# Kernel optimization log

Hardware: AMD Instinct MI355X
Metric: run time of the kernel (lower is better)

Reference implementation:

```python
import jax, jax.numpy as jnp
import numpy as np

N = 50000      # nodes
E = 800000     # edges (before self-loops)
IN = 256       # input features
H = 8          # heads
C = 32         # hidden channels per head
OUT = 40       # classes
NEG_SLOPE = 0.2


def setup_inputs() -> dict:
    key = jax.random.key(0)
    ks = jax.random.split(key, 12)
    sd = lambda k, sh: (jax.random.normal(k, sh, jnp.float32) * 0.05)
    return {
        "x": jax.random.normal(ks[0], (N, IN), jnp.float32),
        "edge_index": jax.random.randint(ks[1], (2, E), 0, N),
        "W1": sd(ks[2], (IN, H * C)),
        "a_src1": sd(ks[3], (H, C)),
        "a_dst1": sd(ks[4], (H, C)),
        "b1": jnp.zeros((C,), jnp.float32),
        "W2": sd(ks[5], (C, H * C)),
        "a_src2": sd(ks[6], (H, C)),
        "a_dst2": sd(ks[7], (H, C)),
        "b2": jnp.zeros((C,), jnp.float32),
        "Wo": sd(ks[8], (C, OUT)),
        "bo": jnp.zeros((OUT,), jnp.float32),
    }


def gat_layer(x, src, dst, n, W, a_src, a_dst, b):
    # x: [N, F]; src/dst: [E'] (self-loops included). concat=False -> mean over heads.
    h = (x @ W).reshape(n, H, C)                       # [N, H, C]
    alpha_src = jnp.sum(h * a_src, axis=-1)            # [N, H]
    alpha_dst = jnp.sum(h * a_dst, axis=-1)            # [N, H]
    e = alpha_src[src] + alpha_dst[dst]                # [E', H]
    e = jnp.where(e > 0, e, NEG_SLOPE * e)             # leaky_relu
    # segment softmax over incoming edges of each dst node
    m = jax.ops.segment_max(e, dst, num_segments=n)    # [N, H]
    ex = jnp.exp(e - m[dst])                           # [E', H]
    s = jax.ops.segment_sum(ex, dst, num_segments=n)   # [N, H]
    alpha = ex / s[dst]                                # [E', H]
    msg = alpha[:, :, None] * h[src]                   # [E', H, C]
    out = jax.ops.segment_sum(msg, dst, num_segments=n)  # [N, H, C]
    return out.mean(axis=1) + b                        # [N, C]


def reference(x, edge_index, W1, a_src1, a_dst1, b1, W2, a_src2, a_dst2, b2, Wo, bo):
    n = x.shape[0]
    loops = jnp.arange(n, dtype=edge_index.dtype)
    src = jnp.concatenate([edge_index[0], loops])      # add self-loops (PyG default)
    dst = jnp.concatenate([edge_index[1], loops])
    h = gat_layer(x, src, dst, n, W1, a_src1, a_dst1, b1)
    h = jax.nn.elu(h)                                  # dropout skipped (eval)
    h = gat_layer(h, src, dst, n, W2, a_src2, a_dst2, b2)
    h = jax.nn.elu(h)
    logits = h @ Wo + bo
    return jax.nn.log_softmax(logits, axis=1)
```

## Files before the change

### kernel.cpp

```cpp
#include <hip/hip_runtime.h>
#include <math.h>

#define N_NODES 50000
#define N_PAD   50016
#define N_EDGES 800000
#define E_TOT   (N_EDGES + N_NODES)
#define F_IN    256
#define NHEAD   8
#define CH      32
#define HC      256
#define OUT_C   40
#define NEG_SLOPE 0.2f
#define CAP     64
#define G_WCVT  ((HC * F_IN + 255) / 256)
#define G_WCVT2 ((HC * CH + 255) / 256)
#define NRANGE  8
#define RANGE_SZ (N_NODES / NRANGE)
#define BIN_CHUNK 2048
#define G_BINCH ((E_TOT + BIN_CHUNK - 1) / BIN_CHUNK)
#define G_BIN   (G_BINCH * NRANGE)

typedef unsigned short u16;
typedef unsigned int   u32;
typedef unsigned char  u8;
typedef __attribute__((ext_vector_type(8))) short bf16x8;
typedef __attribute__((ext_vector_type(4))) float f32x4;
typedef __attribute__((ext_vector_type(2))) float f32x2;

__device__ __forceinline__ u16 f2bf(float f) {
    union { u32 u; float f; } x; x.f = f;
    u32 u = x.u;
    return (u16)((u + 0x7fffu + ((u >> 16) & 1u)) >> 16);
}
__device__ __forceinline__ float bflo(u32 v) {
    union { u32 u; float f; } x; x.u = v << 16; return x.f;
}
__device__ __forceinline__ u8 f2fp8(float f) {
    return (u8)(__builtin_amdgcn_cvt_pk_fp8_f32(f, f, 0, false) & 0xff);
}


__global__ __launch_bounds__(256) void prep_kernel(const int* __restrict__ ei,
        int* __restrict__ cursor, u16* __restrict__ csr_src,
        const float* __restrict__ W1, u16* __restrict__ Wt,
        const float* __restrict__ W2, u16* __restrict__ W2t) {
    int b = blockIdx.x;
    if (b < G_BIN) {
        const int r  = b & (NRANGE - 1);
        const int ch = b >> 3;
        const int lo = r * RANGE_SZ, hi = lo + RANGE_SZ;
        int j0 = ch * BIN_CHUNK + threadIdx.x;
        #pragma unroll
        for (int i = 0; i < BIN_CHUNK / 256; ++i) {
            int j = j0 + i * 256;
            if (j < E_TOT) {
                int d = (j < N_EDGES) ? ei[N_EDGES + j] : (j - N_EDGES);
                if (d >= lo && d < hi) {
                    int s = (j < N_EDGES) ? ei[j] : d;
                    int pos = atomicAdd(&cursor[d], 1);
                    if (pos < CAP) csr_src[d * CAP + pos] = (u16)s;
                }
            }
        }
    } else if (b < G_BIN + G_WCVT) {
        int t = (b - G_BIN) * 256 + threadIdx.x;
        int n = t & 255, k = t >> 8;
        Wt[(size_t)n * F_IN + k] = f2bf(W1[(size_t)k * HC + n]);
    } else {
        int t = (b - G_BIN - G_WCVT) * 256 + threadIdx.x;
        if (t >= HC * CH) return;
        int n = t & 255, k = t >> 8;
        W2t[(size_t)n * CH + k] = f2bf(W2[(size_t)k * HC + n]);
    }
}

__global__ __launch_bounds__(256) void sort_kernel(const int* __restrict__ cursor,
        u16* __restrict__ csr_src) {
    const int dst  = (blockIdx.x * 256 + threadIdx.x) >> 6;
    if (dst >= N_NODES) return;
    const int lane = threadIdx.x & 63;
    const int cnt  = min(cursor[dst], CAP);
    u32 v = (lane < cnt) ? (u32)csr_src[dst * CAP + lane] : 0x7FFFFFFFu;
    #pragma unroll
    for (int k = 2; k <= 64; k <<= 1) {
        #pragma unroll
        for (int j = k >> 1; j > 0; j >>= 1) {
            u32 pv = (u32)__shfl_xor((int)v, j, 64);
            bool asc      = ((lane & k) == 0);
            bool keep_min = (((lane & j) == 0) == asc);
            v = keep_min ? min(v, pv) : max(v, pv);
        }
    }
    if (lane < cnt) csr_src[dst * CAP + lane] = (u16)v;
}

__device__ __forceinline__ void gemm_epilogue(f32x4 acc[2][4], int row0, int quad,
        int l16, int nb, const float* __restrict__ a_src,
        const float* __restrict__ a_dst, u8* __restrict__ ht8,
        float* __restrict__ asrc, float* __restrict__ adst) {
    #pragma unroll
    for (int m = 0; m < 2; ++m) {
        #pragma unroll
        for (int r = 0; r < 4; ++r) {
            int row = row0 + m * 16 + quad * 4 + r;
            if (row < N_NODES) {
                u8* hr = ht8 + (size_t)row * HC;
                #pragma unroll
                for (int n = 0; n < 4; ++n)
                    hr[nb + n * 16 + l16] = f2fp8(acc[m][n][r]);
            }
        }
    }
    const int hA = nb >> 5;
    const float sA0 = a_src[hA * 32 + l16],       sA1 = a_src[hA * 32 + 16 + l16];
    const float sB0 = a_src[(hA + 1) * 32 + l16], sB1 = a_src[(hA + 1) * 32 + 16 + l16];
    const float dA0 = a_dst[hA * 32 + l16],       dA1 = a_dst[hA * 32 + 16 + l16];
    const float dB0 = a_dst[(hA + 1) * 32 + l16], dB1 = a_dst[(hA + 1) * 32 + 16 + l16];
    #pragma unroll
    for (int m = 0; m < 2; ++m) {
        #pragma unroll
        for (int r = 0; r < 4; ++r) {
            float pa = acc[m][0][r] * sA0 + acc[m][1][r] * sA1;
            float pb = acc[m][2][r] * sB0 + acc[m][3][r] * sB1;
            float qa = acc[m][0][r] * dA0 + acc[m][1][r] * dA1;
            float qb = acc[m][2][r] * dB0 + acc[m][3][r] * dB1;
            #pragma unroll
            for (int off = 1; off < 16; off <<= 1) {
                pa += __shfl_xor(pa, off, 64);
                pb += __shfl_xor(pb, off, 64);
                qa += __shfl_xor(qa, off, 64);
                qb += __shfl_xor(qb, off, 64);
            }
            int row = row0 + m * 16 + quad * 4 + r;
            if (l16 == 0 && row < N_NODES) {
                asrc[row * NHEAD + hA]     = pa;
                asrc[row * NHEAD + hA + 1] = pb;
                adst[row * NHEAD + hA]     = qa;
                adst[row * NHEAD + hA + 1] = qb;
            }
        }
    }
}

__global__ __launch_bounds__(256) void gemm1_mfma(const float* __restrict__ x,
        const u16* __restrict__ Wt, const float* __restrict__ a_src,
        const float* __restrict__ a_dst, u8* __restrict__ ht8,
        float* __restrict__ asrc, float* __restrict__ adst) {
    __shared__ u16 As[32 * 256];
    const int row0 = blockIdx.x * 32;
    const int t    = threadIdx.x;

    {
        const int r   = t >> 3;
        const int sub = t & 7;
        const int gr  = min(row0 + r, N_NODES - 1);
        const float4* xr = (const float4*)(x + (size_t)gr * F_IN);
        const int sw = (r & 7) << 4;
        char* Ar = (char*)As + r * 512;
        #pragma unroll
        for (int i = 0; i < 8; ++i) {
            int f4 = i * 8 + sub;
            float4 v = xr[f4];
            u32 lo = (u32)f2bf(v.x) | ((u32)f2bf(v.y) << 16);
            u32 hi = (u32)f2bf(v.z) | ((u32)f2bf(v.w) << 16);
            *(uint2*)(Ar + ((f4 * 8) ^ sw)) = make_uint2(lo, hi);
        }
    }
    __syncthreads();

    const int wave = t >> 6;
    const int lane = t & 63;
    const int l16  = lane & 15;
    const int quad = lane >> 4;
    const int nb   = wave * 64;
    const int swr  = (l16 & 7) << 4;
    const char* Ab = (const char*)As;

    f32x4 acc[2][4];
    #pragma unroll
    for (int m = 0; m < 2; ++m)
        #pragma unroll
        for (int n = 0; n < 4; ++n) acc[m][n] = (f32x4){0.f, 0.f, 0.f, 0.f};

    const u16* bp = Wt + (size_t)(nb + l16) * F_IN;

    #pragma unroll 1
    for (int k0 = 0; k0 < F_IN; k0 += 32) {
        const int ko = k0 + quad * 8;
        bf16x8 a0 = *(const bf16x8*)(Ab + l16 * 512 + ((ko * 2) ^ swr));
        bf16x8 a1 = *(const bf16x8*)(Ab + (16 + l16) * 512 + ((ko * 2) ^ swr));
        bf16x8 b0 = *(const bf16x8*)(bp + 0 * 16 * F_IN + ko);
        bf16x8 b1 = *(const bf16x8*)(bp + 1 * 16 * F_IN + ko);
        bf16x8 b2 = *(const bf16x8*)(bp + 2 * 16 * F_IN + ko);
        bf16x8 b3 = *(const bf16x8*)(bp + 3 * 16 * F_IN + ko);
        acc[0][0] = __builtin_amdgcn_mfma_f32_16x16x32_bf16(a0, b0, acc[0][0], 0, 0, 0);
        acc[0][1] = __builtin_amdgcn_mfma_f32_16x16x32_bf16(a0, b1, acc[0][1], 0, 0, 0);
        acc[0][2] = __builtin_amdgcn_mfma_f32_16x16x32_bf16(a0, b2, acc[0][2], 0, 0, 0);
        acc[0][3] = __builtin_amdgcn_mfma_f32_16x16x32_bf16(a0, b3, acc[0][3], 0, 0, 0);
        acc[1][0] = __builtin_amdgcn_mfma_f32_16x16x32_bf16(a1, b0, acc[1][0], 0, 0, 0);
        acc[1][1] = __builtin_amdgcn_mfma_f32_16x16x32_bf16(a1, b1, acc[1][1], 0, 0, 0);
        acc[1][2] = __builtin_amdgcn_mfma_f32_16x16x32_bf16(a1, b2, acc[1][2], 0, 0, 0);
        acc[1][3] = __builtin_amdgcn_mfma_f32_16x16x32_bf16(a1, b3, acc[1][3], 0, 0, 0);
    }
    gemm_epilogue(acc, row0, quad, l16, nb, a_src, a_dst, ht8, asrc, adst);
}

__global__ __launch_bounds__(256) void gemm2_mfma(const u16* __restrict__ hmb,
        const u16* __restrict__ W2t, const float* __restrict__ a_src,
        const float* __restrict__ a_dst, u8* __restrict__ ht8,
        float* __restrict__ asrc, float* __restrict__ adst) {
    const int row0 = blockIdx.x * 32;
    const int t    = threadIdx.x;
    const int wave = t >> 6;
    const int lane = t & 63;
    const int l16  = lane & 15;
    const int quad = lane >> 4;
    const int nb   = wave * 64;
    const int ko   = quad * 8;

    const u16* a0p = hmb + (size_t)(row0 + l16) * CH;
    const u16* a1p = a0p + 16 * CH;
    const u16* bp  = W2t + (size_t)(nb + l16) * CH;

    bf16x8 a0 = *(const bf16x8*)(a0p + ko);
    bf16x8 a1 = *(const bf16x8*)(a1p + ko);
    bf16x8 b0 = *(const bf16x8*)(bp + 0 * 16 * CH + ko);
    bf16x8 b1 = *(const bf16x8*)(bp + 1 * 16 * CH + ko);
    bf16x8 b2 = *(const bf16x8*)(bp + 2 * 16 * CH + ko);
    bf16x8 b3 = *(const bf16x8*)(bp + 3 * 16 * CH + ko);

    f32x4 z = (f32x4){0.f, 0.f, 0.f, 0.f};
    f32x4 acc[2][4];
    acc[0][0] = __builtin_amdgcn_mfma_f32_16x16x32_bf16(a0, b0, z, 0, 0, 0);
    acc[0][1] = __builtin_amdgcn_mfma_f32_16x16x32_bf16(a0, b1, z, 0, 0, 0);
    acc[0][2] = __builtin_amdgcn_mfma_f32_16x16x32_bf16(a0, b2, z, 0, 0, 0);
    acc[0][3] = __builtin_amdgcn_mfma_f32_16x16x32_bf16(a0, b3, z, 0, 0, 0);
    acc[1][0] = __builtin_amdgcn_mfma_f32_16x16x32_bf16(a1, b0, z, 0, 0, 0);
    acc[1][1] = __builtin_amdgcn_mfma_f32_16x16x32_bf16(a1, b1, z, 0, 0, 0);
    acc[1][2] = __builtin_amdgcn_mfma_f32_16x16x32_bf16(a1, b2, z, 0, 0, 0);
    acc[1][3] = __builtin_amdgcn_mfma_f32_16x16x32_bf16(a1, b3, z, 0, 0, 0);

    gemm_epilogue(acc, row0, quad, l16, nb, a_src, a_dst, ht8, asrc, adst);
}

__global__ __launch_bounds__(256) void attn_kernel(const int* __restrict__ degp,
        const u16* __restrict__ csr_src, const float* __restrict__ asrc,
        const float* __restrict__ adst, const u8* __restrict__ ht8,
        const float* __restrict__ b, u16* __restrict__ out) {
    const int wid = (blockIdx.x * 256 + threadIdx.x) >> 6;
    if (wid >= N_NODES) return;
    const int dst  = wid;
    const int lane = threadIdx.x & 63;
    const int q    = lane >> 4;
    const int l16  = lane & 15;
    const int h    = l16 >> 1;
    const float ad_own = adst[dst * NHEAD + h];
    const u8* hbase = ht8 + l16 * 16;

    f32x2 acc2[8];
    #pragma unroll
    for (int i = 0; i < 8; ++i) acc2[i] = (f32x2){0.f, 0.f};
    float wsum = 0.f;

    const int cnt = min(degp[dst], CAP);
    const int p0 = dst * CAP, p1 = p0 + cnt;
    const int nt = (cnt + 7) >> 3;

    float asA = -1e30f, asB = -1e30f;
    uint4 hvA = make_uint4(0u, 0u, 0u, 0u), hvB = make_uint4(0u, 0u, 0u, 0u);
    int e = p0 + q;
    if (e < p1) {
        int s = (int)csr_src[e];
        asA = asrc[s * NHEAD + h];
        hvA = *(const uint4*)(hbase + ((size_t)s << 8));
    }
    if (e + 4 < p1) {
        int s = (int)csr_src[e + 4];
        asB = asrc[s * NHEAD + h];
        hvB = *(const uint4*)(hbase + ((size_t)s << 8));
    }

    for (int it = 0; it < nt; ++it) {
        float aA = asA; uint4 hA = hvA;
        float aB = asB; uint4 hB = hvB;
        asA = -1e30f; asB = -1e30f;
        if (e + 8 < p1) {
            int s = (int)csr_src[e + 8];
            asA = asrc[s * NHEAD + h];
            hvA = *(const uint4*)(hbase + ((size_t)s << 8));
        }
        if (e + 12 < p1) {
            int s = (int)csr_src[e + 12];
            asB = asrc[s * NHEAD + h];
            hvB = *(const uint4*)(hbase + ((size_t)s << 8));
        }
        {
            float x = aA + ad_own;
            x = x > 0.f ? x : NEG_SLOPE * x;
            float w = __expf(x);
            wsum += w;
            f32x2 w2; w2.x = w; w2.y = w;
            acc2[0] = __builtin_elementwise_fma(w2, __builtin_amdgcn_cvt_pk_f32_fp8(hA.x, false), acc2[0]);
            acc2[1] = __builtin_elementwise_fma(w2, __builtin_amdgcn_cvt_pk_f32_fp8(hA.x, true ), acc2[1]);
            acc2[2] = __builtin_elementwise_fma(w2, __builtin_amdgcn_cvt_pk_f32_fp8(hA.y, false), acc2[2]);
            acc2[3] = __builtin_elementwise_fma(w2, __builtin_amdgcn_cvt_pk_f32_fp8(hA.y, true ), acc2[3]);
            acc2[4] = __builtin_elementwise_fma(w2, __builtin_amdgcn_cvt_pk_f32_fp8(hA.z, false), acc2[4]);
            acc2[5] = __builtin_elementwise_fma(w2, __builtin_amdgcn_cvt_pk_f32_fp8(hA.z, true ), acc2[5]);
            acc2[6] = __builtin_elementwise_fma(w2, __builtin_amdgcn_cvt_pk_f32_fp8(hA.w, false), acc2[6]);
            acc2[7] = __builtin_elementwise_fma(w2, __builtin_amdgcn_cvt_pk_f32_fp8(hA.w, true ), acc2[7]);
        }
        {
            float x = aB + ad_own;
            x = x > 0.f ? x : NEG_SLOPE * x;
            float w = __expf(x);
            wsum += w;
            f32x2 w2; w2.x = w; w2.y = w;
            acc2[0] = __builtin_elementwise_fma(w2, __builtin_amdgcn_cvt_pk_f32_fp8(hB.x, false), acc2[0]);
            acc2[1] = __builtin_elementwise_fma(w2, __builtin_amdgcn_cvt_pk_f32_fp8(hB.x, true ), acc2[1]);
            acc2[2] = __builtin_elementwise_fma(w2, __builtin_amdgcn_cvt_pk_f32_fp8(hB.y, false), acc2[2]);
            acc2[3] = __builtin_elementwise_fma(w2, __builtin_amdgcn_cvt_pk_f32_fp8(hB.y, true ), acc2[3]);
            acc2[4] = __builtin_elementwise_fma(w2, __builtin_amdgcn_cvt_pk_f32_fp8(hB.z, false), acc2[4]);
            acc2[5] = __builtin_elementwise_fma(w2, __builtin_amdgcn_cvt_pk_f32_fp8(hB.z, true ), acc2[5]);
            acc2[6] = __builtin_elementwise_fma(w2, __builtin_amdgcn_cvt_pk_f32_fp8(hB.w, false), acc2[6]);
            acc2[7] = __builtin_elementwise_fma(w2, __builtin_amdgcn_cvt_pk_f32_fp8(hB.w, true ), acc2[7]);
        }
        e += 8;
    }

    #pragma unroll
    for (int i = 0; i < 8; ++i) {
        acc2[i].x += __shfl_xor(acc2[i].x, 16, 64);
        acc2[i].y += __shfl_xor(acc2[i].y, 16, 64);
        acc2[i].x += __shfl_xor(acc2[i].x, 32, 64);
        acc2[i].y += __shfl_xor(acc2[i].y, 32, 64);
    }
    wsum += __shfl_xor(wsum, 16, 64);
    wsum += __shfl_xor(wsum, 32, 64);

    float winv = 1.0f / wsum;
    f32x2 winv2; winv2.x = winv; winv2.y = winv;
    #pragma unroll
    for (int i = 0; i < 8; ++i) acc2[i] *= winv2;

    #pragma unroll
    for (int i = 0; i < 8; ++i) {
        acc2[i].x += __shfl_xor(acc2[i].x, 2, 64);
        acc2[i].y += __shfl_xor(acc2[i].y, 2, 64);
        acc2[i].x += __shfl_xor(acc2[i].x, 4, 64);
        acc2[i].y += __shfl_xor(acc2[i].y, 4, 64);
        acc2[i].x += __shfl_xor(acc2[i].x, 8, 64);
        acc2[i].y += __shfl_xor(acc2[i].y, 8, 64);
    }

    if (lane < 2) {
        const int c0 = lane * 16;
        const float4* bp4 = (const float4*)(b + c0);
        float4 b0 = bp4[0], b1 = bp4[1], b2 = bp4[2], b3 = bp4[3];
        float bb[16] = {b0.x, b0.y, b0.z, b0.w, b1.x, b1.y, b1.z, b1.w,
                        b2.x, b2.y, b2.z, b2.w, b3.x, b3.y, b3.z, b3.w};
        u32 d[8];
        #pragma unroll
        for (int i = 0; i < 8; ++i) {
            float v0 = acc2[i].x * 0.125f + bb[2 * i];
            float v1 = acc2[i].y * 0.125f + bb[2 * i + 1];
            v0 = v0 > 0.f ? v0 : (__expf(v0) - 1.f);
            v1 = v1 > 0.f ? v1 : (__expf(v1) - 1.f);
            d[i] = (u32)f2bf(v0) | ((u32)f2bf(v1) << 16);
        }
        uint4* op = (uint4*)(out + (size_t)dst * CH + c0);
        op[0] = make_uint4(d[0], d[1], d[2], d[3]);
        op[1] = make_uint4(d[4], d[5], d[6], d[7]);
    }
}

__global__ __launch_bounds__(256) void attn_fin_kernel(const int* __restrict__ degp,
        const u16* __restrict__ csr_src, const float* __restrict__ asrc,
        const float* __restrict__ adst, const u8* __restrict__ ht8,
        const float* __restrict__ b, const float* __restrict__ Wo,
        const float* __restrict__ bo, float* __restrict__ out) {
    const int dst  = (blockIdx.x * 256 + threadIdx.x) >> 6;
    const int lane = threadIdx.x & 63;
    const int w4   = threadIdx.x >> 6;
    const int q    = lane >> 4;
    const int l16  = lane & 15;
    const int h    = l16 >> 1;
    const float ad_own = adst[dst * NHEAD + h];
    const u8* hbase = ht8 + l16 * 16;

    __shared__ float hsm[4][CH];

    f32x2 acc2[8];
    #pragma unroll
    for (int i = 0; i < 8; ++i) acc2[i] = (f32x2){0.f, 0.f};
    float wsum = 0.f;

    const int cnt = min(degp[dst], CAP);
    const int p0 = dst * CAP, p1 = p0 + cnt;
    const int nt = (cnt + 7) >> 3;

    float asA = -1e30f, asB = -1e30f;
    uint4 hvA = make_uint4(0u, 0u, 0u, 0u), hvB = make_uint4(0u, 0u, 0u, 0u);
    int e = p0 + q;
    if (e < p1) {
        int s = (int)csr_src[e];
        asA = asrc[s * NHEAD + h];
        hvA = *(const uint4*)(hbase + ((size_t)s << 8));
    }
    if (e + 4 < p1) {
        int s = (int)csr_src[e + 4];
        asB = asrc[s * NHEAD + h];
        hvB = *(const uint4*)(hbase + ((size_t)s << 8));
    }

    for (int it = 0; it < nt; ++it) {
        float aA = asA; uint4 hA = hvA;
        float aB = asB; uint4 hB = hvB;
        asA = -1e30f; asB = -1e30f;
        if (e + 8 < p1) {
            int s = (int)csr_src[e + 8];
            asA = asrc[s * NHEAD + h];
            hvA = *(const uint4*)(hbase + ((size_t)s << 8));
        }
        if (e + 12 < p1) {
            int s = (int)csr_src[e + 12];
            asB = asrc[s * NHEAD + h];
            hvB = *(const uint4*)(hbase + ((size_t)s << 8));
        }
        {
            float x = aA + ad_own;
            x = x > 0.f ? x : NEG_SLOPE * x;
            float w = __expf(x);
            wsum += w;
            f32x2 w2; w2.x = w; w2.y = w;
            acc2[0] = __builtin_elementwise_fma(w2, __builtin_amdgcn_cvt_pk_f32_fp8(hA.x, false), acc2[0]);
            acc2[1] = __builtin_elementwise_fma(w2, __builtin_amdgcn_cvt_pk_f32_fp8(hA.x, true ), acc2[1]);
            acc2[2] = __builtin_elementwise_fma(w2, __builtin_amdgcn_cvt_pk_f32_fp8(hA.y, false), acc2[2]);
            acc2[3] = __builtin_elementwise_fma(w2, __builtin_amdgcn_cvt_pk_f32_fp8(hA.y, true ), acc2[3]);
            acc2[4] = __builtin_elementwise_fma(w2, __builtin_amdgcn_cvt_pk_f32_fp8(hA.z, false), acc2[4]);
            acc2[5] = __builtin_elementwise_fma(w2, __builtin_amdgcn_cvt_pk_f32_fp8(hA.z, true ), acc2[5]);
            acc2[6] = __builtin_elementwise_fma(w2, __builtin_amdgcn_cvt_pk_f32_fp8(hA.w, false), acc2[6]);
            acc2[7] = __builtin_elementwise_fma(w2, __builtin_amdgcn_cvt_pk_f32_fp8(hA.w, true ), acc2[7]);
        }
        {
            float x = aB + ad_own;
            x = x > 0.f ? x : NEG_SLOPE * x;
            float w = __expf(x);
            wsum += w;
            f32x2 w2; w2.x = w; w2.y = w;
            acc2[0] = __builtin_elementwise_fma(w2, __builtin_amdgcn_cvt_pk_f32_fp8(hB.x, false), acc2[0]);
            acc2[1] = __builtin_elementwise_fma(w2, __builtin_amdgcn_cvt_pk_f32_fp8(hB.x, true ), acc2[1]);
            acc2[2] = __builtin_elementwise_fma(w2, __builtin_amdgcn_cvt_pk_f32_fp8(hB.y, false), acc2[2]);
            acc2[3] = __builtin_elementwise_fma(w2, __builtin_amdgcn_cvt_pk_f32_fp8(hB.y, true ), acc2[3]);
            acc2[4] = __builtin_elementwise_fma(w2, __builtin_amdgcn_cvt_pk_f32_fp8(hB.z, false), acc2[4]);
            acc2[5] = __builtin_elementwise_fma(w2, __builtin_amdgcn_cvt_pk_f32_fp8(hB.z, true ), acc2[5]);
            acc2[6] = __builtin_elementwise_fma(w2, __builtin_amdgcn_cvt_pk_f32_fp8(hB.w, false), acc2[6]);
            acc2[7] = __builtin_elementwise_fma(w2, __builtin_amdgcn_cvt_pk_f32_fp8(hB.w, true ), acc2[7]);
        }
        e += 8;
    }

    #pragma unroll
    for (int i = 0; i < 8; ++i) {
        acc2[i].x += __shfl_xor(acc2[i].x, 16, 64);
        acc2[i].y += __shfl_xor(acc2[i].y, 16, 64);
        acc2[i].x += __shfl_xor(acc2[i].x, 32, 64);
        acc2[i].y += __shfl_xor(acc2[i].y, 32, 64);
    }
    wsum += __shfl_xor(wsum, 16, 64);
    wsum += __shfl_xor(wsum, 32, 64);

    float winv = 1.0f / wsum;
    f32x2 winv2; winv2.x = winv; winv2.y = winv;
    #pragma unroll
    for (int i = 0; i < 8; ++i) acc2[i] *= winv2;

    #pragma unroll
    for (int i = 0; i < 8; ++i) {
        acc2[i].x += __shfl_xor(acc2[i].x, 2, 64);
        acc2[i].y += __shfl_xor(acc2[i].y, 2, 64);
        acc2[i].x += __shfl_xor(acc2[i].x, 4, 64);
        acc2[i].y += __shfl_xor(acc2[i].y, 4, 64);
        acc2[i].x += __shfl_xor(acc2[i].x, 8, 64);
        acc2[i].y += __shfl_xor(acc2[i].y, 8, 64);
    }

    if (lane < 2) {
        #pragma unroll
        for (int i = 0; i < 8; ++i) {
            hsm[w4][lane * 16 + 2 * i]     = acc2[i].x * 0.125f;
            hsm[w4][lane * 16 + 2 * i + 1] = acc2[i].y * 0.125f;
        }
    }
    __syncthreads();
    if (lane < CH) {
        float v = hsm[w4][lane] + b[lane];
        hsm[w4][lane] = v > 0.f ? v : (__expf(v) - 1.f);
    }
    __syncthreads();
    float logit = -INFINITY;
    if (lane < OUT_C) {
        float a = bo[lane];
        #pragma unroll
        for (int k = 0; k < CH; ++k) a += hsm[w4][k] * Wo[k * OUT_C + lane];
        logit = a;
    }
    float mx = logit;
    #pragma unroll
    for (int off = 32; off; off >>= 1) mx = fmaxf(mx, __shfl_xor(mx, off, 64));
    float ex = (lane < OUT_C) ? __expf(logit - mx) : 0.f;
    float ss = ex;
    #pragma unroll
    for (int off = 32; off; off >>= 1) ss += __shfl_xor(ss, off, 64);
    if (lane < OUT_C) out[(size_t)dst * OUT_C + lane] = logit - mx - __logf(ss);
}

extern "C" void kernel_launch(void* const* d_in, const int* in_sizes, int n_in,
                              void* d_out, int out_size, void* d_ws, size_t ws_size,
                              hipStream_t stream) {
    const float* x      = (const float*)d_in[0];
    const int*   ei     = (const int*)  d_in[1];
    const float* W1     = (const float*)d_in[2];
    const float* a_src1 = (const float*)d_in[3];
    const float* a_dst1 = (const float*)d_in[4];
    const float* b1     = (const float*)d_in[5];
    const float* W2     = (const float*)d_in[6];
    const float* a_src2 = (const float*)d_in[7];
    const float* a_dst2 = (const float*)d_in[8];
    const float* b2     = (const float*)d_in[9];
    const float* Wo     = (const float*)d_in[10];
    const float* bo     = (const float*)d_in[11];
    float* out = (float*)d_out;

    char* ws = (char*)d_ws;
    size_t off = 0;
    auto carve = [&](size_t bytes) { char* p = ws + off; off += (bytes + 255) & ~(size_t)255; return p; };
    u8*    ht8     = (u8*)   carve((size_t)N_NODES * HC);
    u16*   Wt      = (u16*)  carve((size_t)HC * F_IN * 2);
    u16*   W2t     = (u16*)  carve((size_t)HC * CH * 2);
    float* asrc    = (float*)carve((size_t)N_NODES * NHEAD * 4);
    float* adst    = (float*)carve((size_t)N_NODES * NHEAD * 4);
    u16*   hmid    = (u16*)  carve((size_t)N_PAD * CH * 2);
    int*   cursor  = (int*)  carve((size_t)N_NODES * 4);
    u16*   csr_src = (u16*)  carve((size_t)N_NODES * CAP * 2);

    const int g_prep  = G_BIN + G_WCVT + G_WCVT2;
    const int g_sort  = (N_NODES * 64 + 255) / 256;
    const int g_gemm  = (N_NODES + 31) / 32;
    const int g_attn  = (N_NODES * 64 + 255) / 256;

    (void)hipMemsetAsync(cursor, 0, (size_t)N_NODES * 4, stream);
    prep_kernel<<<g_prep, 256, 0, stream>>>(ei, cursor, csr_src, W1, Wt, W2, W2t);
    sort_kernel<<<g_sort, 256, 0, stream>>>(cursor, csr_src);

    gemm1_mfma<<<g_gemm, 256, 0, stream>>>(x, Wt, a_src1, a_dst1, ht8, asrc, adst);
    attn_kernel<<<g_attn, 256, 0, stream>>>(cursor, csr_src, asrc, adst, ht8, b1, hmid);

    gemm2_mfma<<<g_gemm, 256, 0, stream>>>(hmid, W2t, a_src2, a_dst2, ht8, asrc, adst);
    attn_fin_kernel<<<g_attn, 256, 0, stream>>>(cursor, csr_src, asrc, adst,
                                                ht8, b2, Wo, bo, out);
}
```

Before: 323.9 us.

## Fuse layer-2 projection into layer-1 attention and drop CSR sort pass

Layer-1 attention now finishes each node by applying ELU, multiplying by W2 (converted to bf16 into shared memory per block), and writing fp8 features plus layer-2 attention logits. This removes the separate gemm2 launch and the hmid round trip. The sort kernel is dropped, so neighbors are visited in atomic-insertion order, and the output projection moves to its own small kernel. Every attention block pays for loading and converting the 16 KB W2 into shared memory. Unsorted neighbor order can change gather locality and make float summation order nondeterministic.

After: 325.8 us. About the same (+0.6%).

```diff
diff --git a/kernel.cpp b/kernel.cpp
--- a/kernel.cpp
+++ b/kernel.cpp
@@ -13,12 +13,12 @@
 #define NEG_SLOPE 0.2f
 #define CAP     64
 #define G_WCVT  ((HC * F_IN + 255) / 256)
-#define G_WCVT2 ((HC * CH + 255) / 256)
 #define NRANGE  8
 #define RANGE_SZ (N_NODES / NRANGE)
 #define BIN_CHUNK 2048
 #define G_BINCH ((E_TOT + BIN_CHUNK - 1) / BIN_CHUNK)
 #define G_BIN   (G_BINCH * NRANGE)
+#define G_GEMM  (N_PAD / 32)
 
 typedef unsigned short u16;
 typedef unsigned int   u32;
@@ -42,8 +42,7 @@
 
 __global__ __launch_bounds__(256) void prep_kernel(const int* __restrict__ ei,
         int* __restrict__ cursor, u16* __restrict__ csr_src,
-        const float* __restrict__ W1, u16* __restrict__ Wt,
-        const float* __restrict__ W2, u16* __restrict__ W2t) {
+        const float* __restrict__ W1, u16* __restrict__ Wt) {
     int b = blockIdx.x;
     if (b < G_BIN) {
         const int r  = b & (NRANGE - 1);
@@ -62,36 +61,11 @@
                 }
             }
         }
-    } else if (b < G_BIN + G_WCVT) {
+    } else {
         int t = (b - G_BIN) * 256 + threadIdx.x;
         int n = t & 255, k = t >> 8;
         Wt[(size_t)n * F_IN + k] = f2bf(W1[(size_t)k * HC + n]);
-    } else {
-        int t = (b - G_BIN - G_WCVT) * 256 + threadIdx.x;
-        if (t >= HC * CH) return;
-        int n = t & 255, k = t >> 8;
-        W2t[(size_t)n * CH + k] = f2bf(W2[(size_t)k * HC + n]);
-    }
-}
-
-__global__ __launch_bounds__(256) void sort_kernel(const int* __restrict__ cursor,
-        u16* __restrict__ csr_src) {
-    const int dst  = (blockIdx.x * 256 + threadIdx.x) >> 6;
-    if (dst >= N_NODES) return;
-    const int lane = threadIdx.x & 63;
-    const int cnt  = min(cursor[dst], CAP);
-    u32 v = (lane < cnt) ? (u32)csr_src[dst * CAP + lane] : 0x7FFFFFFFu;
-    #pragma unroll
-    for (int k = 2; k <= 64; k <<= 1) {
-        #pragma unroll
-        for (int j = k >> 1; j > 0; j >>= 1) {
-            u32 pv = (u32)__shfl_xor((int)v, j, 64);
-            bool asc      = ((lane & k) == 0);
-            bool keep_min = (((lane & j) == 0) == asc);
-            v = keep_min ? min(v, pv) : max(v, pv);
-        }
-    }
-    if (lane < cnt) csr_src[dst * CAP + lane] = (u16)v;
+    }
 }
 
 __device__ __forceinline__ void gemm_epilogue(f32x4 acc[2][4], int row0, int quad,
@@ -205,52 +179,39 @@
     gemm_epilogue(acc, row0, quad, l16, nb, a_src, a_dst, ht8, asrc, adst);
 }
 
-__global__ __launch_bounds__(256) void gemm2_mfma(const u16* __restrict__ hmb,
-        const u16* __restrict__ W2t, const float* __restrict__ a_src,
-        const float* __restrict__ a_dst, u8* __restrict__ ht8,
-        float* __restrict__ asrc, float* __restrict__ adst) {
-    const int row0 = blockIdx.x * 32;
-    const int t    = threadIdx.x;
-    const int wave = t >> 6;
-    const int lane = t & 63;
-    const int l16  = lane & 15;
-    const int quad = lane >> 4;
-    const int nb   = wave * 64;
-    const int ko   = quad * 8;
-
-    const u16* a0p = hmb + (size_t)(row0 + l16) * CH;
-    const u16* a1p = a0p + 16 * CH;
-    const u16* bp  = W2t + (size_t)(nb + l16) * CH;
-
-    bf16x8 a0 = *(const bf16x8*)(a0p + ko);
-    bf16x8 a1 = *(const bf16x8*)(a1p + ko);
-    bf16x8 b0 = *(const bf16x8*)(bp + 0 * 16 * CH + ko);
-    bf16x8 b1 = *(const bf16x8*)(bp + 1 * 16 * CH + ko);
-    bf16x8 b2 = *(const bf16x8*)(bp + 2 * 16 * CH + ko);
-    bf16x8 b3 = *(const bf16x8*)(bp + 3 * 16 * CH + ko);
-
-    f32x4 z = (f32x4){0.f, 0.f, 0.f, 0.f};
-    f32x4 acc[2][4];
-    acc[0][0] = __builtin_amdgcn_mfma_f32_16x16x32_bf16(a0, b0, z, 0, 0, 0);
-    acc[0][1] = __builtin_amdgcn_mfma_f32_16x16x32_bf16(a0, b1, z, 0, 0, 0);
-    acc[0][2] = __builtin_amdgcn_mfma_f32_16x16x32_bf16(a0, b2, z, 0, 0, 0);
-    acc[0][3] = __builtin_amdgcn_mfma_f32_16x16x32_bf16(a0, b3, z, 0, 0, 0);
-    acc[1][0] = __builtin_amdgcn_mfma_f32_16x16x32_bf16(a1, b0, z, 0, 0, 0);
-    acc[1][1] = __builtin_amdgcn_mfma_f32_16x16x32_bf16(a1, b1, z, 0, 0, 0);
-    acc[1][2] = __builtin_amdgcn_mfma_f32_16x16x32_bf16(a1, b2, z, 0, 0, 0);
-    acc[1][3] = __builtin_amdgcn_mfma_f32_16x16x32_bf16(a1, b3, z, 0, 0, 0);
-
-    gemm_epilogue(acc, row0, quad, l16, nb, a_src, a_dst, ht8, asrc, adst);
-}
-
-__global__ __launch_bounds__(256) void attn_kernel(const int* __restrict__ degp,
-        const u16* __restrict__ csr_src, const float* __restrict__ asrc,
-        const float* __restrict__ adst, const u8* __restrict__ ht8,
-        const float* __restrict__ b, u16* __restrict__ out) {
-    const int wid = (blockIdx.x * 256 + threadIdx.x) >> 6;
-    if (wid >= N_NODES) return;
-    const int dst  = wid;
+__global__ __launch_bounds__(256) void attn1_fused_kernel(
+        const int* __restrict__ degp, const u16* __restrict__ csr_src,
+        const float* __restrict__ asrc, const float* __restrict__ adst,
+        const u8* __restrict__ ht8, const float* __restrict__ b1,
+        const float* __restrict__ W2, const float* __restrict__ a_src2,
+        const float* __restrict__ a_dst2, u8* __restrict__ ht8b,
+        float* __restrict__ asrc2, float* __restrict__ adst2) {
+    __shared__ u16  W2s[CH * HC];
+    __shared__ float sas2[HC], sad2[HC];
+    __shared__ float bs1[CH];
+    __shared__ float hrow_s[4][CH];
+
+    {
+        for (int i = threadIdx.x; i < CH * HC / 8; i += 256) {
+            const float4* wp = (const float4*)W2 + (size_t)i * 2;
+            float4 v0 = wp[0], v1 = wp[1];
+            u32 p0 = (u32)f2bf(v0.x) | ((u32)f2bf(v0.y) << 16);
+            u32 p1 = (u32)f2bf(v0.z) | ((u32)f2bf(v0.w) << 16);
+            u32 p2 = (u32)f2bf(v1.x) | ((u32)f2bf(v1.y) << 16);
+            u32 p3 = (u32)f2bf(v1.z) | ((u32)f2bf(v1.w) << 16);
+            ((uint4*)W2s)[i] = make_uint4(p0, p1, p2, p3);
+        }
+        if (threadIdx.x < HC) {
+            sas2[threadIdx.x] = a_src2[threadIdx.x];
+            sad2[threadIdx.x] = a_dst2[threadIdx.x];
+        }
+        if (threadIdx.x < CH) bs1[threadIdx.x] = b1[threadIdx.x];
+    }
+    __syncthreads();
+
+    const int dst  = (blockIdx.x * 256 + threadIdx.x) >> 6;
     const int lane = threadIdx.x & 63;
+    const int w4   = threadIdx.x >> 6;
     const int q    = lane >> 4;
     const int l16  = lane & 15;
     const int h    = l16 >> 1;
@@ -336,12 +297,10 @@
     }
     wsum += __shfl_xor(wsum, 16, 64);
     wsum += __shfl_xor(wsum, 32, 64);
-
     float winv = 1.0f / wsum;
     f32x2 winv2; winv2.x = winv; winv2.y = winv;
     #pragma unroll
     for (int i = 0; i < 8; ++i) acc2[i] *= winv2;
-
     #pragma unroll
     for (int i = 0; i < 8; ++i) {
         acc2[i].x += __shfl_xor(acc2[i].x, 2, 64);
@@ -354,40 +313,60 @@
 
     if (lane < 2) {
         const int c0 = lane * 16;
-        const float4* bp4 = (const float4*)(b + c0);
-        float4 b0 = bp4[0], b1 = bp4[1], b2 = bp4[2], b3 = bp4[3];
-        float bb[16] = {b0.x, b0.y, b0.z, b0.w, b1.x, b1.y, b1.z, b1.w,
-                        b2.x, b2.y, b2.z, b2.w, b3.x, b3.y, b3.z, b3.w};
-        u32 d[8];
         #pragma unroll
         for (int i = 0; i < 8; ++i) {
-            float v0 = acc2[i].x * 0.125f + bb[2 * i];
-            float v1 = acc2[i].y * 0.125f + bb[2 * i + 1];
+            float v0 = acc2[i].x * 0.125f + bs1[c0 + 2 * i];
+            float v1 = acc2[i].y * 0.125f + bs1[c0 + 2 * i + 1];
             v0 = v0 > 0.f ? v0 : (__expf(v0) - 1.f);
             v1 = v1 > 0.f ? v1 : (__expf(v1) - 1.f);
-            d[i] = (u32)f2bf(v0) | ((u32)f2bf(v1) << 16);
-        }
-        uint4* op = (uint4*)(out + (size_t)dst * CH + c0);
-        op[0] = make_uint4(d[0], d[1], d[2], d[3]);
-        op[1] = make_uint4(d[4], d[5], d[6], d[7]);
-    }
-}
-
-__global__ __launch_bounds__(256) void attn_fin_kernel(const int* __restrict__ degp,
+            hrow_s[w4][c0 + 2 * i]     = v0;
+            hrow_s[w4][c0 + 2 * i + 1] = v1;
+        }
+    }
+
+    float o0 = 0.f, o1 = 0.f, o2 = 0.f, o3 = 0.f;
+    const u16* wb = W2s + lane * 4;
+    #pragma unroll
+    for (int k = 0; k < CH; ++k) {
+        uint2 wv = *(const uint2*)(wb + k * HC);
+        float hk = hrow_s[w4][k];
+        o0 += hk * bflo(wv.x & 0xffffu);
+        o1 += hk * bflo(wv.x >> 16);
+        o2 += hk * bflo(wv.y & 0xffffu);
+        o3 += hk * bflo(wv.y >> 16);
+    }
+
+    u32 lo = __builtin_amdgcn_cvt_pk_fp8_f32(o0, o1, 0, false) & 0xffffu;
+    u32 hi = __builtin_amdgcn_cvt_pk_fp8_f32(o2, o3, 0, false) & 0xffffu;
+    *(u32*)(ht8b + (size_t)dst * HC + lane * 4) = lo | (hi << 16);
+
+    const int h2 = lane >> 3;
+    const float* s2 = sas2 + h2 * CH + (lane & 7) * 4;
+    const float* d2 = sad2 + h2 * CH + (lane & 7) * 4;
+    float pa = o0 * s2[0] + o1 * s2[1] + o2 * s2[2] + o3 * s2[3];
+    float qa = o0 * d2[0] + o1 * d2[1] + o2 * d2[2] + o3 * d2[3];
+    pa += __shfl_xor(pa, 1, 64); qa += __shfl_xor(qa, 1, 64);
+    pa += __shfl_xor(pa, 2, 64); qa += __shfl_xor(qa, 2, 64);
+    pa += __shfl_xor(pa, 4, 64); qa += __shfl_xor(qa, 4, 64);
+    if ((lane & 7) == 0) {
+        asrc2[dst * NHEAD + h2] = pa;
+        adst2[dst * NHEAD + h2] = qa;
+    }
+}
+
+__global__ __launch_bounds__(256) void attn_kernel(const int* __restrict__ degp,
         const u16* __restrict__ csr_src, const float* __restrict__ asrc,
         const float* __restrict__ adst, const u8* __restrict__ ht8,
-        const float* __restrict__ b, const float* __restrict__ Wo,
-        const float* __restrict__ bo, float* __restrict__ out) {
-    const int dst  = (blockIdx.x * 256 + threadIdx.x) >> 6;
+        const float* __restrict__ b, u16* __restrict__ out) {
+    const int wid = (blockIdx.x * 256 + threadIdx.x) >> 6;
+    if (wid >= N_NODES) return;
+    const int dst  = wid;
     const int lane = threadIdx.x & 63;
-    const int w4   = threadIdx.x >> 6;
     const int q    = lane >> 4;
     const int l16  = lane & 15;
     const int h    = l16 >> 1;
     const float ad_own = adst[dst * NHEAD + h];
     const u8* hbase = ht8 + l16 * 16;
-
-    __shared__ float hsm[4][CH];
 
     f32x2 acc2[8];
     #pragma unroll
@@ -485,33 +464,51 @@
     }
 
     if (lane < 2) {
+        const int c0 = lane * 16;
+        const float4* bp4 = (const float4*)(b + c0);
+        float4 b0 = bp4[0], b1 = bp4[1], b2 = bp4[2], b3 = bp4[3];
+        float bb[16] = {b0.x, b0.y, b0.z, b0.w, b1.x, b1.y, b1.z, b1.w,
+                        b2.x, b2.y, b2.z, b2.w, b3.x, b3.y, b3.z, b3.w};
+        u32 d[8];
         #pragma unroll
         for (int i = 0; i < 8; ++i) {
-            hsm[w4][lane * 16 + 2 * i]     = acc2[i].x * 0.125f;
-            hsm[w4][lane * 16 + 2 * i + 1] = acc2[i].y * 0.125f;
-        }
-    }
+            float v0 = acc2[i].x * 0.125f + bb[2 * i];
+            float v1 = acc2[i].y * 0.125f + bb[2 * i + 1];
+            v0 = v0 > 0.f ? v0 : (__expf(v0) - 1.f);
+            v1 = v1 > 0.f ? v1 : (__expf(v1) - 1.f);
+            d[i] = (u32)f2bf(v0) | ((u32)f2bf(v1) << 16);
+        }
+        uint4* op = (uint4*)(out + (size_t)dst * CH + c0);
+        op[0] = make_uint4(d[0], d[1], d[2], d[3]);
+        op[1] = make_uint4(d[4], d[5], d[6], d[7]);
+    }
+}
+
+__global__ __launch_bounds__(256) void out_kernel(const u16* __restrict__ hf,
+        const float* __restrict__ Wo, const float* __restrict__ bo,
+        float* __restrict__ out) {
+    const int wave = threadIdx.x >> 6;
+    const int lane = threadIdx.x & 63;
+    const int n    = blockIdx.x * 4 + wave;
+    __shared__ float hs[4][CH];
+    if (n < N_NODES && lane < CH) hs[wave][lane] = bflo((u32)hf[n * CH + lane]);
     __syncthreads();
-    if (lane < CH) {
-        float v = hsm[w4][lane] + b[lane];
-        hsm[w4][lane] = v > 0.f ? v : (__expf(v) - 1.f);
-    }
-    __syncthreads();
+    if (n >= N_NODES) return;
     float logit = -INFINITY;
     if (lane < OUT_C) {
         float a = bo[lane];
         #pragma unroll
-        for (int k = 0; k < CH; ++k) a += hsm[w4][k] * Wo[k * OUT_C + lane];
+        for (int k = 0; k < CH; ++k) a += hs[wave][k] * Wo[k * OUT_C + lane];
         logit = a;
     }
-    float mx = logit;
-    #pragma unroll
-    for (int off = 32; off; off >>= 1) mx = fmaxf(mx, __shfl_xor(mx, off, 64));
-    float ex = (lane < OUT_C) ? __expf(logit - mx) : 0.f;
-    float ss = ex;
-    #pragma unroll
-    for (int off = 32; off; off >>= 1) ss += __shfl_xor(ss, off, 64);
-    if (lane < OUT_C) out[(size_t)dst * OUT_C + lane] = logit - mx - __logf(ss);
+    float m = logit;
+    #pragma unroll
+    for (int off = 32; off; off >>= 1) m = fmaxf(m, __shfl_xor(m, off, 64));
+    float ex = (lane < OUT_C) ? __expf(logit - m) : 0.f;
+    float ssum = ex;
+    #pragma unroll
+    for (int off = 32; off; off >>= 1) ssum += __shfl_xor(ssum, off, 64);
+    if (lane < OUT_C) out[(size_t)n * OUT_C + lane] = logit - m - __logf(ssum);
 }
 
 extern "C" void kernel_launch(void* const* d_in, const int* in_sizes, int n_in,
@@ -534,28 +531,31 @@
     char* ws = (char*)d_ws;
     size_t off = 0;
     auto carve = [&](size_t bytes) { char* p = ws + off; off += (bytes + 255) & ~(size_t)255; return p; };
-    u8*    ht8     = (u8*)   carve((size_t)N_NODES * HC);
+    u8*    ht8a    = (u8*)   carve((size_t)N_NODES * HC);
+    u8*    ht8b    = (u8*)   carve((size_t)N_NODES * HC);
     u16*   Wt      = (u16*)  carve((size_t)HC * F_IN * 2);
-    u16*   W2t     = (u16*)  carve((size_t)HC * CH * 2);
     float* asrc    = (float*)carve((size_t)N_NODES * NHEAD * 4);
     float* adst    = (float*)carve((size_t)N_NODES * NHEAD * 4);
-    u16*   hmid    = (u16*)  carve((size_t)N_PAD * CH * 2);
+    float* asrc2   = (float*)carve((size_t)N_NODES * NHEAD * 4);
+    float* adst2   = (float*)carve((size_t)N_NODES * NHEAD * 4);
+    u16*   hout    = (u16*)  carve((size_t)N_NODES * CH * 2);
     int*   cursor  = (int*)  carve((size_t)N_NODES * 4);
     u16*   csr_src = (u16*)  carve((size_t)N_NODES * CAP * 2);
 
-    const int g_prep  = G_BIN + G_WCVT + G_WCVT2;
-    const int g_sort  = (N_NODES * 64 + 255) / 256;
-    const int g_gemm  = (N_NODES + 31) / 32;
+    const int g_prep  = G_BIN + G_WCVT;
     const int g_attn  = (N_NODES * 64 + 255) / 256;
+    const int g_out   = (N_NODES + 3) / 4;
 
     (void)hipMemsetAsync(cursor, 0, (size_t)N_NODES * 4, stream);
-    prep_kernel<<<g_prep, 256, 0, stream>>>(ei, cursor, csr_src, W1, Wt, W2, W2t);
-    sort_kernel<<<g_sort, 256, 0, stream>>>(cursor, csr_src);
-
-    gemm1_mfma<<<g_gemm, 256, 0, stream>>>(x, Wt, a_src1, a_dst1, ht8, asrc, adst);
-    attn_kernel<<<g_attn, 256, 0, stream>>>(cursor, csr_src, asrc, adst, ht8, b1, hmid);
-
-    gemm2_mfma<<<g_gemm, 256, 0, stream>>>(hmid, W2t, a_src2, a_dst2, ht8, asrc, adst);
-    attn_fin_kernel<<<g_attn, 256, 0, stream>>>(cursor, csr_src, asrc, adst,
-                                                ht8, b2, Wo, bo, out);
-}
+    prep_kernel<<<g_prep, 256, 0, stream>>>(ei, cursor, csr_src, W1, Wt);
+
+    gemm1_mfma<<<G_GEMM, 256, 0, stream>>>(x, Wt, a_src1, a_dst1, ht8a, asrc, adst);
+    attn1_fused_kernel<<<g_attn, 256, 0, stream>>>(cursor, csr_src, asrc, adst,
+                                                   ht8a, b1, W2, a_src2, a_dst2,
+                                                   ht8b, asrc2, adst2);
+
+    attn_kernel<<<g_attn, 256, 0, stream>>>(cursor, csr_src, asrc2, adst2,
+                                            ht8b, b2, hout);
+
+    out_kernel<<<g_out, 256, 0, stream>>>(hout, Wo, bo, out);
+}
```
